# Kernel optimization log

Measured on AMD Instinct MI355X. Metric: run time of the kernel, lower is better.

The kernel has to match this reference:

```python
import jax, jax.numpy as jnp
import numpy as np

TOPK, NUM_CLASSES = 13, 80
ALPHA, BETA, GAMMA, EPS = 1.0, 5.0, 3.0, 1e-09


def _make_boxes(key, shape, img=640.0, wmin=10.0, wmax=120.0):
    k1, k2 = jax.random.split(key)
    cxy = jax.random.uniform(k1, shape[:-1] + (2,), minval=0.0, maxval=img)
    wh = jax.random.uniform(k2, shape[:-1] + (2,), minval=wmin, maxval=wmax)
    return jnp.concatenate([cxy - wh / 2, cxy + wh / 2], axis=-1)


def setup_inputs() -> dict:
    key = jax.random.key(0)
    ks = jax.random.split(key, 7)
    bs, A, C, n = 16, 8400, 80, 60
    return {
        'pd_scores': jax.random.uniform(ks[0], (bs, A, C), dtype=jnp.float32),
        'pd_bboxes': _make_boxes(ks[1], (bs, A, 4)),
        'pd_angles': jax.random.uniform(ks[2], (bs, A, 1), minval=0.0, maxval=90.0),
        'anc_points': jax.random.uniform(ks[3], (A, 2), minval=0.0, maxval=640.0),
        'gt_labels': jax.random.randint(ks[4], (bs, n, 1), 0, C, dtype=jnp.int32),
        'gt_bboxes': _make_boxes(ks[5], (bs, n, 4)),
        'gt_angles': jax.random.uniform(ks[6], (bs, n, 1), minval=0.0, maxval=90.0),
        'mask_gt': jnp.ones((bs, n, 1), jnp.float32),
        'epoch_num': 1,
    }


def _cos_fn(x, ar, beta=2.0):
    return 0.5 + 0.5 * jnp.cos(beta / ar * x / 180.0 * jnp.pi + jnp.pi * (1.0 - beta / (2.0 * ar)))


def _angle_measure(pd_angles, gt_angles, gt_bboxes):
    # gt area ratio w/h -> (bs, n, 1, 1)
    w = gt_bboxes[..., 2:3] - gt_bboxes[..., 0:1]
    h = gt_bboxes[..., 3:4] - gt_bboxes[..., 1:2]
    ar = (w / (h + 1e-05))[:, :, None, :]
    theta = jnp.abs(gt_angles[:, :, None, :] - pd_angles[:, None, :, :])  # (bs,n,A,1)
    av = 1.0 / ar / (2.0 - 1.0 / ar)
    mx = _cos_fn(0.0, ar)
    mn = _cos_fn(90.0, ar)
    r = (_cos_fn(theta, ar) - mn) / (mx - mn) * (1.0 - av) + av
    r = jnp.where(jnp.isnan(r), 0.0, r)
    return jnp.squeeze(r, -1)  # (bs, n, A)


def _pairwise_iou(gt, pd):
    # gt (bs,n,4), pd (bs,A,4) -> (bs,n,A)
    lt = jnp.maximum(gt[:, :, None, :2], pd[:, None, :, :2])
    rb = jnp.minimum(gt[:, :, None, 2:], pd[:, None, :, 2:])
    inter = jnp.clip(rb - lt, 0.0).prod(-1)
    a1 = jnp.clip(gt[..., 2:] - gt[..., :2], 0.0).prod(-1)[:, :, None]
    a2 = jnp.clip(pd[..., 2:] - pd[..., :2], 0.0).prod(-1)[:, None, :]
    return inter / (a1 + a2 - inter + EPS)


def _select_topk(metrics, topk_mask):
    bs, n, A = metrics.shape
    _, idxs = jax.lax.top_k(metrics, TOPK)
    idxs = jnp.where(topk_mask, idxs, 0)
    flat = idxs.reshape(bs * n, TOPK)
    cnt = jnp.zeros((bs * n, A), jnp.int32).at[jnp.arange(bs * n)[:, None], flat].add(1)
    cnt = cnt.reshape(bs, n, A)
    return jnp.where(cnt > 1, 0, cnt).astype(metrics.dtype)


def _select_highest_overlaps(mask_pos, overlaps, n):
    fg = mask_pos.sum(-2)                                   # (bs, A)
    multi = fg[:, None, :] > 1                              # (bs, 1, A)
    is_max = jax.nn.one_hot(overlaps.argmax(1), n, axis=1, dtype=mask_pos.dtype)  # (bs,n,A)
    mask_pos = jnp.where(multi, is_max, mask_pos)
    fg = mask_pos.sum(-2)
    tgt_idx = mask_pos.argmax(-2)                           # (bs, A)
    return tgt_idx, fg, mask_pos


def reference(pd_scores, pd_bboxes, pd_angles, anc_points, gt_labels, gt_bboxes, gt_angles, mask_gt, epoch_num):
    bs, A, C = pd_scores.shape
    n = gt_bboxes.shape[1]
    lab = gt_labels[..., 0].astype(jnp.int32)               # (bs, n)

    # bbox_scores: pd_scores[b, :, gt_label] -> (bs, n, A)
    pts = jnp.transpose(pd_scores, (0, 2, 1))               # (bs, C, A)
    bbox_scores = jnp.take_along_axis(pts, lab[:, :, None], axis=1)

    overlaps = _pairwise_iou(gt_bboxes, pd_bboxes)          # (bs, n, A)
    ang = _angle_measure(pd_angles, gt_angles, gt_bboxes)   # (bs, n, A)
    align = bbox_scores ** ALPHA * overlaps ** BETA * ang ** GAMMA

    # anchors-inside-gt mask (bs, n, A)
    lt = anc_points[None, None, :, :] - gt_bboxes[:, :, None, :2]
    rb = gt_bboxes[:, :, None, 2:] - anc_points[None, None, :, :]
    in_gts = (jnp.concatenate([lt, rb], -1).min(-1) > EPS).astype(align.dtype)

    topk_mask = jnp.broadcast_to(mask_gt > 0, (bs, n, TOPK))
    mask_topk = _select_topk(align * in_gts, topk_mask)
    mask_pos = mask_topk * in_gts * mask_gt                 # (bs, n, A)

    tgt_idx, fg, mask_pos = _select_highest_overlaps(mask_pos, overlaps, n)

    # gather per-anchor targets from flattened gt tensors
    off = tgt_idx + jnp.arange(bs, dtype=tgt_idx.dtype)[:, None] * n   # (bs, A)
    tlab = lab.reshape(-1)[off]
    tlab = jnp.where(tlab < 0, 0, tlab)
    tbb = gt_bboxes.reshape(-1, 4)[off]                     # (bs, A, 4)
    tang = gt_angles.reshape(-1, 1)[off]                    # (bs, A, 1)
    ts = jax.nn.one_hot(tlab, C, dtype=pd_scores.dtype)     # (bs, A, C)
    ts = jnp.where(fg[:, :, None] > 0, ts, 0.0)

    # normalized alignment metric scaling
    align = align * mask_pos
    pam = align.max(-1, keepdims=True)                      # (bs, n, 1)
    pov = (overlaps * mask_pos).max(-1, keepdims=True)      # (bs, n, 1)
    norm = (align * pov / (pam + EPS)).max(-2)[:, :, None]  # (bs, A, 1)
    ts = ts * norm

    return tlab, tbb, tang, ts, fg > 0
```

## Files before the change

kernel.cpp:

```cpp
#include <hip/hip_runtime.h>
#include <math.h>

#define TOPK 13
#define PI_F 3.14159265358979323846f
#define RPB 4
#define CAP 64

typedef unsigned int u32;
typedef unsigned long long u64;

__device__ __forceinline__ u32 ford(float f) {
    u32 u = __float_as_uint(f);
    return (u & 0x80000000u) ? ~u : (u | 0x80000000u);
}
__device__ __forceinline__ float funord(u32 o) {
    u32 u = (o & 0x80000000u) ? (o & 0x7FFFFFFFu) : ~o;
    return __uint_as_float(u);
}

__device__ __forceinline__ float iou_fn(float4 g, float4 p) {
    float ltx = fmaxf(g.x, p.x), lty = fmaxf(g.y, p.y);
    float rbx = fminf(g.z, p.z), rby = fminf(g.w, p.w);
    float inter = fmaxf(rbx - ltx, 0.0f) * fmaxf(rby - lty, 0.0f);
    float a1 = fmaxf(g.z - g.x, 0.0f) * fmaxf(g.w - g.y, 0.0f);
    float a2 = fmaxf(p.z - p.x, 0.0f) * fmaxf(p.w - p.y, 0.0f);
    return inter / (((a1 + a2) - inter) + 1e-9f);
}

struct RowParams { float av, bar, offc, mx, mn; };

__device__ __forceinline__ RowParams row_params(float4 g) {
    float w = g.z - g.x, h = g.w - g.y;
    float ar = w / (h + 1e-5f);
    float ia = 1.0f / ar;
    RowParams rp;
    rp.av = ia / (2.0f - ia);
    rp.bar = 2.0f / ar;
    rp.offc = PI_F * (1.0f - 2.0f / (2.0f * ar));
    rp.mx = 0.5f + 0.5f * cosf(rp.offc);
    rp.mn = 0.5f + 0.5f * cosf(rp.bar * 90.0f / 180.0f * PI_F + rp.offc);
    return rp;
}

__device__ __forceinline__ float ang_measure(const RowParams& rp, float theta) {
    float cfv = 0.5f + 0.5f * cosf(rp.bar * theta / 180.0f * PI_F + rp.offc);
    float r = (cfv - rp.mn) / (rp.mx - rp.mn) * (1.0f - rp.av) + rp.av;
    return isnan(r) ? 0.0f : r;
}

__device__ __forceinline__ float align_fn(float s, float iou, float r) {
    float iou2 = iou * iou;
    float iou5 = (iou2 * iou2) * iou;
    float r3 = (r * r) * r;
    return (s * iou5) * r3;
}

__global__ void k0_init(int* cnt, int* assign1, u32* pam, u32* pov, int BA, int BN) {
    int t = blockIdx.x * blockDim.x + threadIdx.x;
    if (t < BA) { cnt[t] = 0; assign1[t] = -1; }
    if (t < BN) { pam[t] = 0x80000000u; pov[t] = 0x80000000u; }
}

__global__ __launch_bounds__(256)
void k1_topk(const float* __restrict__ scores, const float* __restrict__ pbox,
             const float* __restrict__ pang, const float* __restrict__ anc,
             const int* __restrict__ glab, const float* __restrict__ gbox,
             const float* __restrict__ gang, const float* __restrict__ mgt,
             int* __restrict__ cnt, int* __restrict__ assign1,
             float* __restrict__ out,
             int bs, int A, int n, int C) {
    int j = blockIdx.x;
    int b = j % bs;
    int rg = j / bs;
    int i0 = rg * RPB;
    int tid = threadIdx.x;
    int BA = bs * A;

    int nF4 = BA * (C / 4);
    int zCH = (nF4 + gridDim.x - 1) / gridDim.x;
    int zBeg = j * zCH + tid;
    int zEnd = min(j * zCH + zCH, nF4);
    float4* tsf4 = (float4*)(out + (size_t)BA * 6);
    const float4 z4 = make_float4(0.0f, 0.0f, 0.0f, 0.0f);

    __shared__ u64 posL[RPB][CAP];
    __shared__ u64 zdump[RPB][256];
    __shared__ int pc[RPB];
    __shared__ int ovfrows[RPB];
    __shared__ int novf;
    __shared__ u64 red[4];

    if (tid < RPB) pc[tid] = 0;
    if (tid == 0) novf = 0;

    float4 g[RPB];
    float rpav[RPB], rpbar[RPB], rpoff[RPB], rpmx[RPB], rpmn[RPB];
    float ga[RPB];
    int lab[RPB];
    bool act[RPB];
#pragma unroll
    for (int r = 0; r < RPB; ++r) {
        int i = i0 + r;
        act[r] = false;
        g[r] = make_float4(0.0f, 0.0f, 0.0f, 0.0f);
        ga[r] = 0.0f; lab[r] = 0;
        rpav[r] = rpbar[r] = rpoff[r] = rpmx[r] = rpmn[r] = 0.0f;
        if (i < n) {
            int bi = b * n + i;
            if (mgt[bi] > 0.0f) {
                act[r] = true;
                g[r] = ((const float4*)gbox)[bi];
                RowParams rp = row_params(g[r]);
                rpav[r] = rp.av; rpbar[r] = rp.bar; rpoff[r] = rp.offc;
                rpmx[r] = rp.mx; rpmn[r] = rp.mn;
                ga[r] = gang[bi];
                lab[r] = glab[bi];
            }
        }
    }
    __syncthreads();

    const float4* pb = ((const float4*)pbox) + (size_t)b * A;
    const float* pa = pang + (size_t)b * A;
    const float2* ac = (const float2*)anc;
    const float* scb = scores + (size_t)b * A * C;

    u64 zkey[RPB];
#pragma unroll
    for (int r = 0; r < RPB; ++r) zkey[r] = 0ull;

    int a = tid;
    float4 p = pb[a];
    float pav = pa[a];
    float2 apt = ac[a];

    int nit = (A + 255) >> 8;
    int clampA = A - 1;
    for (int it = 0; it < nit; ++it) {
        int an = a + 256;
        int can = min(an, clampA);
        float4 p2 = pb[can];
        float pav2 = pa[can];
        float2 apt2 = ac[can];
        if (zBeg < zEnd) { tsf4[zBeg] = z4; zBeg += 256; }
        if (zBeg < zEnd) { tsf4[zBeg] = z4; zBeg += 256; }
        if (a < A) {
#pragma unroll
            for (int r = 0; r < RPB; ++r) {
                if (!act[r]) continue;
                float mnv = fminf(fminf(apt.x - g[r].x, apt.y - g[r].y),
                                  fminf(g[r].z - apt.x, g[r].w - apt.y));
                float iou = iou_fn(g[r], p);
                bool na = (mnv > 1e-9f) && (iou > 0.0f);
                if (na || zkey[r] == 0ull) {
                    RowParams rp;
                    rp.av = rpav[r]; rp.bar = rpbar[r]; rp.offc = rpoff[r];
                    rp.mx = rpmx[r]; rp.mn = rpmn[r];
                    float th = fabsf(ga[r] - pav);
                    float rr = ang_measure(rp, th);
                    bool zc;
                    if (na && rr > 0.0f) {
                        float s = scb[(size_t)a * C + lab[r]];
                        float v = align_fn(s, iou, rr);
                        if (v > 0.0f) {
                            zc = false;
                            u64 key = ((u64)ford(v) << 32) | (u64)(0xFFFFFFFFu - (u32)a);
                            int idx = atomicAdd(&pc[r], 1);
                            if (idx < CAP) posL[r][idx] = key;
                        } else zc = true;
                    } else zc = (rr >= 0.0f);
                    if (zc && zkey[r] == 0ull)
                        zkey[r] = (0x80000000ull << 32) | (u64)(0xFFFFFFFFu - (u32)a);
                }
            }
        }
        a = an; p = p2; pav = pav2; apt = apt2;
    }
    for (; zBeg < zEnd; zBeg += 256) tsf4[zBeg] = z4;

#pragma unroll
    for (int r = 0; r < RPB; ++r) zdump[r][tid] = zkey[r];
    __syncthreads();

    int lane = tid & 63, wv = tid >> 6;

#define MERGE_ROW(RR)                                                          \
    {                                                                          \
        if (act[RR]) {                                                         \
            int P = pc[RR];                                                    \
            if (P <= CAP) {                                                    \
                u64 s0 = (lane < P) ? posL[RR][lane] : 0ull;                   \
                u64 s1 = zdump[RR][lane];                                      \
                u64 s2 = zdump[RR][lane + 64];                                 \
                u64 s3 = zdump[RR][lane + 128];                                \
                u64 s4 = zdump[RR][lane + 192];                                \
                for (int round = 0; round < TOPK; ++round) {                   \
                    u64 m = s0;                                                \
                    if (s1 > m) m = s1;                                        \
                    if (s2 > m) m = s2;                                        \
                    if (s3 > m) m = s3;                                        \
                    if (s4 > m) m = s4;                                        \
                    for (int st = 32; st > 0; st >>= 1) {                      \
                        u64 o = __shfl_xor(m, st, 64);                         \
                        if (o > m) m = o;                                      \
                    }                                                          \
                    if (m == 0ull) break;                                      \
                    bool own = false;                                          \
                    if (s0 == m) { s0 = 0ull; own = true; }                    \
                    else if (s1 == m) { s1 = 0ull; own = true; }               \
                    else if (s2 == m) { s2 = 0ull; own = true; }               \
                    else if (s3 == m) { s3 = 0ull; own = true; }               \
                    else if (s4 == m) { s4 = 0ull; own = true; }               \
                    if (own) {                                                 \
                        int aa = (int)(0xFFFFFFFFu - (u32)(m & 0xFFFFFFFFull));\
                        float2 ap2 = ac[aa];                                   \
                        float mnw = fminf(fminf(ap2.x - g[RR].x,               \
                                                ap2.y - g[RR].y),              \
                                          fminf(g[RR].z - ap2.x,               \
                                                g[RR].w - ap2.y));             \
                        if (mnw > 1e-9f) {                                     \
                            atomicAdd(&cnt[(size_t)b * A + aa], 1);            \
                            atomicMax(&assign1[(size_t)b * A + aa], i0 + RR);  \
                        }                                                      \
                    }                                                          \
                }                                                              \
            } else if (lane == 0) {                                            \
                int o = atomicAdd(&novf, 1);                                   \
                ovfrows[o] = RR;                                               \
            }                                                                  \
        }                                                                      \
    }

    if (wv == 0) MERGE_ROW(0)
    else if (wv == 1) MERGE_ROW(1)
    else if (wv == 2) MERGE_ROW(2)
    else MERGE_ROW(3)
#undef MERGE_ROW
    __syncthreads();

    for (int k = 0; k < novf; ++k) {
        int rI = ovfrows[k];
        int i = i0 + rI;
        int bi = b * n + i;
        float4 gg = ((const float4*)gbox)[bi];
        RowParams rpp = row_params(gg);
        float gga = gang[bi];
        int ll = glab[bi];
        u64 last = 0xFFFFFFFFFFFFFFFFull;
        for (int round = 0; round < TOPK; ++round) {
            u64 best = 0ull;
            for (int aa = tid; aa < A; aa += 256) {
                float2 ap2 = ac[aa];
                float4 pp = pb[aa];
                float mnv = fminf(fminf(ap2.x - gg.x, ap2.y - gg.y),
                                  fminf(gg.z - ap2.x, gg.w - ap2.y));
                float iou = iou_fn(gg, pp);
                bool na = (mnv > 1e-9f) && (iou > 0.0f);
                float th = fabsf(gga - pa[aa]);
                float rr = ang_measure(rpp, th);
                u64 zk = (0x80000000ull << 32) | (u64)(0xFFFFFFFFu - (u32)aa);
                u64 key = 0ull;
                if (na && rr > 0.0f) {
                    float s = scb[(size_t)aa * C + ll];
                    float v = align_fn(s, iou, rr);
                    key = (v > 0.0f)
                        ? (((u64)ford(v) << 32) | (u64)(0xFFFFFFFFu - (u32)aa))
                        : zk;
                } else if (rr >= 0.0f) key = zk;
                if (key < last && key > best) best = key;
            }
            u64 m = best;
            for (int st = 32; st > 0; st >>= 1) {
                u64 o = __shfl_xor(m, st, 64);
                if (o > m) m = o;
            }
            if (lane == 0) red[wv] = m;
            __syncthreads();
            u64 win = red[0];
            if (red[1] > win) win = red[1];
            if (red[2] > win) win = red[2];
            if (red[3] > win) win = red[3];
            __syncthreads();
            if (win == 0ull) break;
            int aw = (int)(0xFFFFFFFFu - (u32)(win & 0xFFFFFFFFull));
            if ((aw & 255) == tid) {
                float2 ap2 = ac[aw];
                float mnw = fminf(fminf(ap2.x - gg.x, ap2.y - gg.y),
                                  fminf(gg.z - ap2.x, gg.w - ap2.y));
                if (mnw > 1e-9f) {
                    atomicAdd(&cnt[(size_t)b * A + aw], 1);
                    atomicMax(&assign1[(size_t)b * A + aw], i);
                }
            }
            last = win;
        }
    }
}

__global__ __launch_bounds__(256)
void k2_resolve(const float* __restrict__ scores, const float* __restrict__ pbox,
                const float* __restrict__ pang, const int* __restrict__ glab,
                const float* __restrict__ gbox, const float* __restrict__ gang,
                const int* __restrict__ cnt, const int* __restrict__ assign1,
                int* __restrict__ assign, float* __restrict__ alignv,
                u32* __restrict__ pam, u32* __restrict__ pov,
                int bs, int A, int n, int C) {
    int t = blockIdx.x * blockDim.x + threadIdx.x;
    if (t >= bs * A) return;
    int b = t / A;
    int c = cnt[t];
    int asg = -1;
    float alv = 0.0f;
    if (c > 0) {
        float4 p = ((const float4*)pbox)[t];
        if (c == 1) {
            asg = assign1[t];
        } else {
            float best = -1.0f;
            asg = 0;
            for (int i = 0; i < n; i++) {
                float4 gi = ((const float4*)gbox)[b * n + i];
                float io = iou_fn(gi, p);
                if (io > best) { best = io; asg = i; }
            }
        }
        float4 g = ((const float4*)gbox)[b * n + asg];
        RowParams rp = row_params(g);
        float iou = iou_fn(g, p);
        float th = fabsf(gang[b * n + asg] - pang[t]);
        float r = ang_measure(rp, th);
        float s = scores[(size_t)t * C + glab[b * n + asg]];
        alv = align_fn(s, iou, r);
        atomicMax(&pam[b * n + asg], ford(alv));
        atomicMax(&pov[b * n + asg], ford(iou));
    }
    assign[t] = asg;
    alignv[t] = alv;
}

__global__ __launch_bounds__(256)
void k3_out(const int* __restrict__ glab, const float* __restrict__ gbox,
            const float* __restrict__ gang, const int* __restrict__ assign,
            const float* __restrict__ alignv, const u32* __restrict__ pam,
            const u32* __restrict__ pov, float* __restrict__ out,
            int bs, int A, int n, int C) {
    int t = blockIdx.x * blockDim.x + threadIdx.x;
    int BA = bs * A;
    if (t >= BA) return;
    int b = t / A;
    int asg = assign[t];
    bool fg = asg >= 0;
    int tgt = fg ? asg : 0;
    int lb = glab[b * n + tgt];
    if (lb < 0) lb = 0;

    out[t] = (float)lb;
    ((float4*)(out + BA))[t] = ((const float4*)gbox)[b * n + tgt];
    out[(size_t)BA * 5 + t] = gang[b * n + tgt];
    out[(size_t)BA * 6 + (size_t)BA * C + t] = fg ? 1.0f : 0.0f;

    if (fg) {
        float pamv = funord(pam[b * n + asg]);
        float povv = funord(pov[b * n + asg]);
        float vv = (alignv[t] * povv) / (pamv + 1e-9f);
        out[(size_t)BA * 6 + (size_t)t * C + lb] = fmaxf(vv, 0.0f);
    }
}

extern "C" void kernel_launch(void* const* d_in, const int* in_sizes, int n_in,
                              void* d_out, int out_size, void* d_ws, size_t ws_size,
                              hipStream_t stream) {
    const float* scores = (const float*)d_in[0];
    const float* pbox = (const float*)d_in[1];
    const float* pang = (const float*)d_in[2];
    const float* anc = (const float*)d_in[3];
    const int* glab = (const int*)d_in[4];
    const float* gbox = (const float*)d_in[5];
    const float* gang = (const float*)d_in[6];
    const float* mgt = (const float*)d_in[7];

    const int C = 80;
    int A = in_sizes[3] / 2;
    int bs = in_sizes[0] / (A * C);
    int n = in_sizes[4] / bs;
    int BA = bs * A;
    int BN = bs * n;

    char* ws = (char*)d_ws;
    int* cnt = (int*)ws;        ws += sizeof(int) * (size_t)BA;
    int* assign1 = (int*)ws;    ws += sizeof(int) * (size_t)BA;
    int* assign = (int*)ws;     ws += sizeof(int) * (size_t)BA;
    float* alignv = (float*)ws; ws += sizeof(float) * (size_t)BA;
    u32* pam = (u32*)ws;        ws += sizeof(u32) * (size_t)BN;
    u32* pov = (u32*)ws;        ws += sizeof(u32) * (size_t)BN;

    int NG = (n + RPB - 1) / RPB;

    k0_init<<<(BA + 255) / 256, 256, 0, stream>>>(cnt, assign1, pam, pov, BA, BN);
    k1_topk<<<bs * NG, 256, 0, stream>>>(scores, pbox, pang, anc, glab, gbox, gang, mgt,
                                         cnt, assign1, (float*)d_out, bs, A, n, C);
    k2_resolve<<<(BA + 255) / 256, 256, 0, stream>>>(scores, pbox, pang, glab, gbox, gang,
                                                     cnt, assign1, assign, alignv, pam, pov,
                                                     bs, A, n, C);
    k3_out<<<(BA + 255) / 256, 256, 0, stream>>>(glab, gbox, gang, assign, alignv, pam, pov,
                                                 (float*)d_out, bs, A, n, C);
}
```

Measured before the change: 174.9 us.

## Split top-k anchor scan into chunks with separate merge kernel

The top-k kernel now splits the anchor dimension into four chunks, so each block computes a partial top-13 per gt row over a quarter of the anchors and writes it to a workspace list. A new small merge kernel combines the per-chunk candidates per gt row and performs the count/assign atomics. This quadruples the grid size, which was only bs*15 blocks, to improve GPU occupancy. The cost is an extra kernel launch, an extra workspace round trip, and the overflow path now runs per wave within its chunk.

```diff
diff --git a/kernel.cpp b/kernel.cpp
--- a/kernel.cpp
+++ b/kernel.cpp
@@ -4,6 +4,7 @@
 #define TOPK 13
 #define PI_F 3.14159265358979323846f
 #define RPB 4
+#define NC 4
 #define CAP 64
 
 typedef unsigned int u32;
@@ -66,12 +67,14 @@
              const float* __restrict__ pang, const float* __restrict__ anc,
              const int* __restrict__ glab, const float* __restrict__ gbox,
              const float* __restrict__ gang, const float* __restrict__ mgt,
-             int* __restrict__ cnt, int* __restrict__ assign1,
-             float* __restrict__ out,
+             u64* __restrict__ wslist, float* __restrict__ out,
              int bs, int A, int n, int C) {
     int j = blockIdx.x;
     int b = j % bs;
-    int rg = j / bs;
+    int r2 = j / bs;
+    int NG = (n + RPB - 1) / RPB;
+    int rg = r2 % NG;
+    int c0 = r2 / NG;
     int i0 = rg * RPB;
     int tid = threadIdx.x;
     int BA = bs * A;
@@ -86,12 +89,7 @@
     __shared__ u64 posL[RPB][CAP];
     __shared__ u64 zdump[RPB][256];
     __shared__ int pc[RPB];
-    __shared__ int ovfrows[RPB];
-    __shared__ int novf;
-    __shared__ u64 red[4];
-
     if (tid < RPB) pc[tid] = 0;
-    if (tid == 0) novf = 0;
 
     float4 g[RPB];
     float rpav[RPB], rpbar[RPB], rpoff[RPB], rpmx[RPB], rpmn[RPB];
@@ -125,26 +123,30 @@
     const float2* ac = (const float2*)anc;
     const float* scb = scores + (size_t)b * A * C;
 
+    int CS = (A + NC - 1) / NC;
+    int start = c0 * CS;
+    int end = min(start + CS, A);
+    int clampE = end - 1;
+
     u64 zkey[RPB];
 #pragma unroll
     for (int r = 0; r < RPB; ++r) zkey[r] = 0ull;
 
-    int a = tid;
+    int a = start + tid;
     float4 p = pb[a];
     float pav = pa[a];
     float2 apt = ac[a];
 
-    int nit = (A + 255) >> 8;
-    int clampA = A - 1;
+    int nit = (end - start + 255) >> 8;
     for (int it = 0; it < nit; ++it) {
         int an = a + 256;
-        int can = min(an, clampA);
+        int can = min(an, clampE);
         float4 p2 = pb[can];
         float pav2 = pa[can];
         float2 apt2 = ac[can];
         if (zBeg < zEnd) { tsf4[zBeg] = z4; zBeg += 256; }
         if (zBeg < zEnd) { tsf4[zBeg] = z4; zBeg += 256; }
-        if (a < A) {
+        if (a < end) {
 #pragma unroll
             for (int r = 0; r < RPB; ++r) {
                 if (!act[r]) continue;
@@ -187,6 +189,7 @@
 #define MERGE_ROW(RR)                                                          \
     {                                                                          \
         if (act[RR]) {                                                         \
+            u64* dst = wslist + ((size_t)(b * n + i0 + RR) * NC + c0) * TOPK;  \
             int P = pc[RR];                                                    \
             if (P <= CAP) {                                                    \
                 u64 s0 = (lane < P) ? posL[RR][lane] : 0ull;                   \
@@ -204,95 +207,104 @@
                         u64 o = __shfl_xor(m, st, 64);                         \
                         if (o > m) m = o;                                      \
                     }                                                          \
-                    if (m == 0ull) break;                                      \
-                    bool own = false;                                          \
-                    if (s0 == m) { s0 = 0ull; own = true; }                    \
-                    else if (s1 == m) { s1 = 0ull; own = true; }               \
-                    else if (s2 == m) { s2 = 0ull; own = true; }               \
-                    else if (s3 == m) { s3 = 0ull; own = true; }               \
-                    else if (s4 == m) { s4 = 0ull; own = true; }               \
-                    if (own) {                                                 \
-                        int aa = (int)(0xFFFFFFFFu - (u32)(m & 0xFFFFFFFFull));\
+                    if (lane == 0) dst[round] = m;                             \
+                    if (m != 0ull) {                                           \
+                        if (s0 == m) s0 = 0ull;                                \
+                        else if (s1 == m) s1 = 0ull;                           \
+                        else if (s2 == m) s2 = 0ull;                           \
+                        else if (s3 == m) s3 = 0ull;                           \
+                        else if (s4 == m) s4 = 0ull;                           \
+                    }                                                          \
+                }                                                              \
+            } else {                                                           \
+                   \
+                u64 last = 0xFFFFFFFFFFFFFFFFull;                              \
+                for (int round = 0; round < TOPK; ++round) {                   \
+                    u64 best = 0ull;                                           \
+                    for (int aa = start + lane; aa < end; aa += 64) {          \
                         float2 ap2 = ac[aa];                                   \
-                        float mnw = fminf(fminf(ap2.x - g[RR].x,               \
+                        float4 pp = pb[aa];                                    \
+                        float mnv = fminf(fminf(ap2.x - g[RR].x,               \
                                                 ap2.y - g[RR].y),              \
                                           fminf(g[RR].z - ap2.x,               \
                                                 g[RR].w - ap2.y));             \
-                        if (mnw > 1e-9f) {                                     \
-                            atomicAdd(&cnt[(size_t)b * A + aa], 1);            \
-                            atomicMax(&assign1[(size_t)b * A + aa], i0 + RR);  \
-                        }                                                      \
+                        float iou = iou_fn(g[RR], pp);                         \
+                        bool na = (mnv > 1e-9f) && (iou > 0.0f);               \
+                        RowParams rp;                                          \
+                        rp.av = rpav[RR]; rp.bar = rpbar[RR];                  \
+                        rp.offc = rpoff[RR];                                   \
+                        rp.mx = rpmx[RR]; rp.mn = rpmn[RR];                    \
+                        float th = fabsf(ga[RR] - pa[aa]);                     \
+                        float rr = ang_measure(rp, th);                        \
+                        u64 zk = (0x80000000ull << 32) |                       \
+                                 (u64)(0xFFFFFFFFu - (u32)aa);                 \
+                        u64 key = 0ull;                                        \
+                        if (na && rr > 0.0f) {                                 \
+                            float s = scb[(size_t)aa * C + lab[RR]];           \
+                            float v = align_fn(s, iou, rr);                    \
+                            key = (v > 0.0f)                                   \
+                                ? (((u64)ford(v) << 32) |                      \
+                                   (u64)(0xFFFFFFFFu - (u32)aa))               \
+                                : zk;                                          \
+                        } else if (rr >= 0.0f) { key = zk; }                   \
+                        if (key < last && key > best) best = key;              \
                     }                                                          \
+                    u64 m = best;                                              \
+                    for (int st = 32; st > 0; st >>= 1) {                      \
+                        u64 o = __shfl_xor(m, st, 64);                         \
+                        if (o > m) m = o;                                      \
+                    }                                                          \
+                    if (lane == 0) dst[round] = m;                             \
+                    last = m;                                                  \
                 }                                                              \
-            } else if (lane == 0) {                                            \
-                int o = atomicAdd(&novf, 1);                                   \
-                ovfrows[o] = RR;                                               \
             }                                                                  \
         }                                                                      \
     }
 
-    if (wv == 0) MERGE_ROW(0)
-    else if (wv == 1) MERGE_ROW(1)
-    else if (wv == 2) MERGE_ROW(2)
-    else MERGE_ROW(3)
+    if (wv == 0) { MERGE_ROW(0) }
+    else if (wv == 1) { MERGE_ROW(1) }
+    else if (wv == 2) { MERGE_ROW(2) }
+    else { MERGE_ROW(3) }
 #undef MERGE_ROW
-    __syncthreads();
-
-    for (int k = 0; k < novf; ++k) {
-        int rI = ovfrows[k];
-        int i = i0 + rI;
-        int bi = b * n + i;
-        float4 gg = ((const float4*)gbox)[bi];
-        RowParams rpp = row_params(gg);
-        float gga = gang[bi];
-        int ll = glab[bi];
-        u64 last = 0xFFFFFFFFFFFFFFFFull;
-        for (int round = 0; round < TOPK; ++round) {
-            u64 best = 0ull;
-            for (int aa = tid; aa < A; aa += 256) {
-                float2 ap2 = ac[aa];
-                float4 pp = pb[aa];
-                float mnv = fminf(fminf(ap2.x - gg.x, ap2.y - gg.y),
-                                  fminf(gg.z - ap2.x, gg.w - ap2.y));
-                float iou = iou_fn(gg, pp);
-                bool na = (mnv > 1e-9f) && (iou > 0.0f);
-                float th = fabsf(gga - pa[aa]);
-                float rr = ang_measure(rpp, th);
-                u64 zk = (0x80000000ull << 32) | (u64)(0xFFFFFFFFu - (u32)aa);
-                u64 key = 0ull;
-                if (na && rr > 0.0f) {
-                    float s = scb[(size_t)aa * C + ll];
-                    float v = align_fn(s, iou, rr);
-                    key = (v > 0.0f)
-                        ? (((u64)ford(v) << 32) | (u64)(0xFFFFFFFFu - (u32)aa))
-                        : zk;
-                } else if (rr >= 0.0f) key = zk;
-                if (key < last && key > best) best = key;
+}
+
+__global__ __launch_bounds__(64)
+void k1m_merge(const float* __restrict__ anc, const float* __restrict__ gbox,
+               const float* __restrict__ mgt, const u64* __restrict__ wslist,
+               int* __restrict__ cnt, int* __restrict__ assign1,
+               int bs, int A, int n) {
+    int j = blockIdx.x;
+    int b = j % bs;
+    int i = j / bs;
+    int bi = b * n + i;
+    if (!(mgt[bi] > 0.0f)) return;
+    int lane = threadIdx.x;
+
+    const int NK = NC * TOPK;
+    const u64* src = wslist + (size_t)bi * NK;
+    u64 ka = (lane < NK) ? src[lane] : 0ull;
+
+    float4 g = ((const float4*)gbox)[bi];
+    const float2* ac = (const float2*)anc;
+
+    for (int round = 0; round < TOPK; round++) {
+        u64 m = ka;
+#pragma unroll
+        for (int st = 32; st > 0; st >>= 1) {
+            u64 o = __shfl_xor(m, st, 64);
+            if (o > m) m = o;
+        }
+        if (m == 0ull) break;
+        if (ka == m) {
+            ka = 0ull;
+            int aa = (int)(0xFFFFFFFFu - (u32)(m & 0xFFFFFFFFull));
+            float2 apt = ac[aa];
+            float mnv = fminf(fminf(apt.x - g.x, apt.y - g.y),
+                              fminf(g.z - apt.x, g.w - apt.y));
+            if (mnv > 1e-9f) {
+                atomicAdd(&cnt[(size_t)b * A + aa], 1);
+                atomicMax(&assign1[(size_t)b * A + aa], i);
             }
-            u64 m = best;
-            for (int st = 32; st > 0; st >>= 1) {
-                u64 o = __shfl_xor(m, st, 64);
-                if (o > m) m = o;
-            }
-            if (lane == 0) red[wv] = m;
-            __syncthreads();
-            u64 win = red[0];
-            if (red[1] > win) win = red[1];
-            if (red[2] > win) win = red[2];
-            if (red[3] > win) win = red[3];
-            __syncthreads();
-            if (win == 0ull) break;
-            int aw = (int)(0xFFFFFFFFu - (u32)(win & 0xFFFFFFFFull));
-            if ((aw & 255) == tid) {
-                float2 ap2 = ac[aw];
-                float mnw = fminf(fminf(ap2.x - gg.x, ap2.y - gg.y),
-                                  fminf(gg.z - ap2.x, gg.w - ap2.y));
-                if (mnw > 1e-9f) {
-                    atomicAdd(&cnt[(size_t)b * A + aw], 1);
-                    atomicMax(&assign1[(size_t)b * A + aw], i);
-                }
-            }
-            last = win;
         }
     }
 }
@@ -387,6 +399,7 @@
     int BN = bs * n;
 
     char* ws = (char*)d_ws;
+    u64* wslist = (u64*)ws;     ws += sizeof(u64) * (size_t)BN * NC * TOPK;
     int* cnt = (int*)ws;        ws += sizeof(int) * (size_t)BA;
     int* assign1 = (int*)ws;    ws += sizeof(int) * (size_t)BA;
     int* assign = (int*)ws;     ws += sizeof(int) * (size_t)BA;
@@ -397,8 +410,9 @@
     int NG = (n + RPB - 1) / RPB;
 
     k0_init<<<(BA + 255) / 256, 256, 0, stream>>>(cnt, assign1, pam, pov, BA, BN);
-    k1_topk<<<bs * NG, 256, 0, stream>>>(scores, pbox, pang, anc, glab, gbox, gang, mgt,
-                                         cnt, assign1, (float*)d_out, bs, A, n, C);
+    k1_topk<<<bs * NG * NC, 256, 0, stream>>>(scores, pbox, pang, anc, glab, gbox, gang,
+                                              mgt, wslist, (float*)d_out, bs, A, n, C);
+    k1m_merge<<<BN, 64, 0, stream>>>(anc, gbox, mgt, wslist, cnt, assign1, bs, A, n);
     k2_resolve<<<(BA + 255) / 256, 256, 0, stream>>>(scores, pbox, pang, glab, gbox, gang,
                                                      cnt, assign1, assign, alignv, pam, pov,
                                                      bs, A, n, C);
```

Measured after the change: 173.8 us. About the same (-0.6%).
